# Optimization experiments

Hardware: AMD Instinct MI355X
Metric: run time of the kernel (lower is better)

Reference implementation:

```python
import jax, jax.numpy as jnp
import numpy as np

DEPTH = 8
EMBED = 1280
HEADS = 16
HD = EMBED // HEADS          # 80
MLP = 4 * EMBED              # 5120
HIDDEN = 3584
MERGE = 2
PATCH_DIM = 3 * 2 * 14 * 14  # 1176
THETA = 10000.0


def _layer_norm(x, g, b, eps=1e-6):
    m = jnp.mean(x, -1, keepdims=True)
    v = jnp.mean((x - m) ** 2, -1, keepdims=True)
    return (x - m) * jax.lax.rsqrt(v + eps) * g + b


def _rotate_half(x):
    h = x.shape[-1] // 2
    return jnp.concatenate([-x[..., h:], x[..., :h]], axis=-1)


def _rope_tables(t, h, w):
    # Spatial-merge-ordered h/w position ids (static python ints -> numpy).
    m = MERGE
    hp = np.broadcast_to(np.arange(h)[:, None], (h, w))
    hp = hp.reshape(h // m, m, w // m, m).transpose(0, 2, 1, 3).reshape(-1)
    wp = np.broadcast_to(np.arange(w)[None, :], (h, w))
    wp = wp.reshape(h // m, m, w // m, m).transpose(0, 2, 1, 3).reshape(-1)
    pos = np.tile(np.stack([hp, wp], axis=-1), (t, 1))  # (seq, 2)
    dim = HD // 2
    inv = 1.0 / (THETA ** (np.arange(0, dim, 2, dtype=np.float32) / dim))  # (dim//2,)
    full = np.arange(max(h, w), dtype=np.float32)[:, None] * inv[None, :]  # (max, dim//2)
    emb = full[pos].reshape(pos.shape[0], dim)          # (seq, HD//2)
    emb = np.concatenate([emb, emb], axis=-1)            # (seq, HD)
    return jnp.asarray(np.cos(emb)), jnp.asarray(np.sin(emb))


def setup_inputs() -> dict:
    key = jax.random.key(0)
    ks = jax.random.split(key, 8)
    seq = 1 * 32 * 32
    s = 0.02
    def n(k, shape):
        return jax.random.normal(k, shape, jnp.float32) * s
    return {
        "x": jax.random.normal(ks[0], (seq, PATCH_DIM), jnp.float32),
        "patch_w": n(ks[1], (PATCH_DIM, EMBED)),
        "ln1_g": jnp.ones((DEPTH, EMBED)), "ln1_b": jnp.zeros((DEPTH, EMBED)),
        "qkv_w": n(ks[2], (DEPTH, EMBED, 3 * EMBED)), "qkv_b": jnp.zeros((DEPTH, 3 * EMBED)),
        "proj_w": n(ks[3], (DEPTH, EMBED, EMBED)), "proj_b": jnp.zeros((DEPTH, EMBED)),
        "ln2_g": jnp.ones((DEPTH, EMBED)), "ln2_b": jnp.zeros((DEPTH, EMBED)),
        "fc1_w": n(ks[4], (DEPTH, EMBED, MLP)), "fc1_b": jnp.zeros((DEPTH, MLP)),
        "fc2_w": n(ks[5], (DEPTH, MLP, EMBED)), "fc2_b": jnp.zeros((DEPTH, EMBED)),
        "mln_g": jnp.ones((EMBED,)), "mln_b": jnp.zeros((EMBED,)),
        "mfc1_w": n(ks[6], (EMBED * MERGE ** 2, EMBED * MERGE ** 2)),
        "mfc1_b": jnp.zeros((EMBED * MERGE ** 2,)),
        "mfc2_w": n(ks[7], (EMBED * MERGE ** 2, HIDDEN)),
        "mfc2_b": jnp.zeros((HIDDEN,)),
        "grid_t": 1, "grid_h": 32, "grid_w": 32,
    }


def reference(x, patch_w, ln1_g, ln1_b, qkv_w, qkv_b, proj_w, proj_b,
              ln2_g, ln2_b, fc1_w, fc1_b, fc2_w, fc2_b,
              mln_g, mln_b, mfc1_w, mfc1_b, mfc2_w, mfc2_b,
              grid_t, grid_h, grid_w):
    seq = x.shape[0]
    cos, sin = _rope_tables(int(grid_t), int(grid_h), int(grid_w))  # (seq, HD)
    # Conv3D with kernel == stride == full patch window is a linear projection.
    h = x @ patch_w  # (seq, EMBED)

    def block(h, p):
        l1g, l1b, qw, qb, pw, pb, l2g, l2b, f1w, f1b, f2w, f2b = p
        y = _layer_norm(h, l1g, l1b)
        qkv = (y @ qw + qb).reshape(seq, 3, HEADS, HD)
        q, k, v = qkv[:, 0], qkv[:, 1], qkv[:, 2]  # (seq, HEADS, HD)
        c, si = cos[:, None, :], sin[:, None, :]
        q = q * c + _rotate_half(q) * si
        k = k * c + _rotate_half(k) * si
        attn = jnp.einsum('shd,thd->hst', q, k) * (HD ** -0.5)
        attn = jax.nn.softmax(attn.astype(jnp.float32), axis=-1).astype(h.dtype)
        o = jnp.einsum('hst,thd->shd', attn, v).reshape(seq, EMBED)
        h = h + o @ pw + pb
        y = _layer_norm(h, l2g, l2b)
        y = y @ f1w + f1b
        y = y * jax.nn.sigmoid(1.702 * y)  # quick_gelu
        h = h + y @ f2w + f2b
        return h, None

    h, _ = jax.lax.scan(
        block, h,
        (ln1_g, ln1_b, qkv_w, qkv_b, proj_w, proj_b,
         ln2_g, ln2_b, fc1_w, fc1_b, fc2_w, fc2_b))

    # Patch merger: LN -> group MERGE^2 tokens -> MLP.
    h = _layer_norm(h, mln_g, mln_b)
    h = h.reshape(seq // MERGE ** 2, EMBED * MERGE ** 2)
    h = jax.nn.gelu(h @ mfc1_w + mfc1_b, approximate=True)
    return h @ mfc2_w + mfc2_b  # (seq//4, HIDDEN)
```

## Files before the change

kernel.cpp:

```cpp
#include <hip/hip_runtime.h>
#include <hip/hip_bf16.h>
#include <cmath>

#define SEQ 1024
#define EMBED 1280
#define HEADS 16
#define HD 80
#define HDP 96
#define MLP_DIM 5120
#define HIDDEN 3584
#define QKV3 3840
#define PATCH_DIMS 1176
#define PATCH_PAD 1184
#define DEPTH 8
#define MSEQ 256
#define MDIM 5120
#define KVSPLIT 4

typedef short short8 __attribute__((ext_vector_type(8)));
typedef short short4v __attribute__((ext_vector_type(4)));
typedef float f32x4 __attribute__((ext_vector_type(4)));

#define GLOAD16(g, l)                                                          \
  __builtin_amdgcn_global_load_lds(                                            \
      (const __attribute__((address_space(1))) void*)(g),                      \
      (__attribute__((address_space(3))) void*)(l), 16, 0, 0)

__device__ __forceinline__ float bf2f(unsigned short u) {
  union { unsigned int i; float f; } x;
  x.i = ((unsigned int)u) << 16;
  return x.f;
}
__device__ __forceinline__ unsigned short f2bf(float f) {
  union { float f; unsigned int i; } x;
  x.f = f;
  unsigned int r = x.i + 0x7fffu + ((x.i >> 16) & 1u);
  return (unsigned short)(r >> 16);
}

__device__ inline float waveReduceSum(float v) {
#pragma unroll
  for (int o = 32; o; o >>= 1) v += __shfl_xor(v, o);
  return v;
}

__global__ void rope_tables_kernel(const int* gh_p, const int* gw_p,
                                   float* __restrict__ cosT, float* __restrict__ sinT) {
  int s = blockIdx.x;
  int j = threadIdx.x;
  if (j >= 40) return;
  int gh = *gh_p, gw = *gw_p;
  int f = s % (gh * gw);
  int d0 = f & 1;
  int b = (f >> 1) & 1;
  int rest = f >> 2;
  int W2 = gw >> 1;
  int c = rest % W2;
  int a = rest / W2;
  int hpos = a * 2 + b;
  int wpos = c * 2 + d0;
  int jp = j % 20;
  float inv = powf(10000.0f, -(2.0f * (float)jp) / 40.0f);
  float val = (float)(j < 20 ? hpos : wpos) * inv;
  cosT[s * 40 + j] = cosf(val);
  sinT[s * 40 + j] = sinf(val);
}

__global__ __launch_bounds__(256) void transpose_w(
    const float* __restrict__ W, int ldW, long long wstep,
    unsigned short* __restrict__ Wt, long long tstep, int Ksrc, int Kpad) {
  __shared__ float t[32][132];
  W += (long long)blockIdx.z * wstep;
  Wt += (long long)blockIdx.z * tstep;
  int k0 = blockIdx.x << 7, n0 = blockIdx.y << 5;
#pragma unroll
  for (int i = 0; i < 4; ++i) {
    int flat = threadIdx.x + (i << 8);
    int r = flat >> 3, c4 = (flat & 7) << 2;
    float4 v = make_float4(0.f, 0.f, 0.f, 0.f);
    if (k0 + r < Ksrc) v = *(const float4*)&W[(long long)(k0 + r) * ldW + n0 + c4];
    t[c4][r] = v.x;
    t[c4 + 1][r] = v.y;
    t[c4 + 2][r] = v.z;
    t[c4 + 3][r] = v.w;
  }
  __syncthreads();
  int n = threadIdx.x >> 3, kb = (threadIdx.x & 7) << 2;
#pragma unroll
  for (int j = 0; j < 4; ++j) {
    int k = kb + (j << 5);
    if (k0 + k < Kpad) {
      short4v o;
      o[0] = (short)f2bf(t[n][k]);
      o[1] = (short)f2bf(t[n][k + 1]);
      o[2] = (short)f2bf(t[n][k + 2]);
      o[3] = (short)f2bf(t[n][k + 3]);
      *(short4v*)&Wt[(long long)(n0 + n) * Kpad + k0 + k] = o;
    }
  }
}

__global__ __launch_bounds__(256) void convert_x(const float* __restrict__ x,
                                                 unsigned short* __restrict__ xb) {
  int idx = blockIdx.x * 256 + threadIdx.x;
  if (idx >= SEQ * PATCH_PAD) return;
  int j = idx % PATCH_PAD, s = idx / PATCH_PAD;
  xb[idx] = (j < PATCH_DIMS) ? f2bf(x[(long long)s * PATCH_DIMS + j]) : 0;
}

__global__ __launch_bounds__(256) void gemm_sk(
    const unsigned short* __restrict__ A, int lda,
    const unsigned short* __restrict__ Bt, int ldb,
    void* __restrict__ outp, const float* __restrict__ bias,
    int M, int N, int K, int chunk, int mode) {
  __shared__ short As[128 * 32];
  __shared__ short Bs[128 * 32];
  int nbx = gridDim.x, nby = gridDim.y, nbz = gridDim.z;
  int orig = blockIdx.x + nbx * (blockIdx.y + nby * blockIdx.z);
  int nwg = nbx * nby * nbz;
  int q = nwg >> 3, r = nwg & 7;
  int xcd = orig & 7, pos = orig >> 3;
  int lid = (xcd < r ? xcd * (q + 1) : r * (q + 1) + (xcd - r) * q) + pos;
  int bx = lid % nbx;
  int tt = lid / nbx;
  int by = tt % nby;
  int bz = tt / nby;

  int bm = by << 7, bn = bx << 7;
  int k0 = bz * chunk;
  int kend = min(K, k0 + chunk);
  int tid = threadIdx.x;
  int lane = tid & 63, wid = tid >> 6;
  int wr = wid >> 1, wc = wid & 1;
  f32x4 acc[4][4] = {};

  int arow = (wid << 4) + (lane >> 2);
  int kblk = (lane & 3) << 3;
  const unsigned short* ga = A + (long long)(bm + arow) * lda + k0 + kblk;
  const unsigned short* gb = Bt + (long long)(bn + arow) * ldb + k0 + kblk;
  short* la = &As[arow * 32 + kblk];
  short* lb = &Bs[arow * 32 + kblk];
  long long stepA = 64LL * lda, stepB = 64LL * ldb;

  int l15 = lane & 15, kb8 = (lane >> 4) << 3;
  int rowA = (wr << 6) + l15;
  int rowB = (wc << 6) + l15;

  for (int k = k0; k < kend; k += 32) {
    __syncthreads();
    GLOAD16(ga, la);
    GLOAD16(ga + stepA, la + 64 * 32);
    GLOAD16(gb, lb);
    GLOAD16(gb + stepB, lb + 64 * 32);
    ga += 32;
    gb += 32;
    __syncthreads();
    short8 af[4], bfr[4];
#pragma unroll
    for (int m = 0; m < 4; ++m)
      af[m] = *(const short8*)&As[(rowA + (m << 4)) * 32 + kb8];
#pragma unroll
    for (int n = 0; n < 4; ++n)
      bfr[n] = *(const short8*)&Bs[(rowB + (n << 4)) * 32 + kb8];
#pragma unroll
    for (int m = 0; m < 4; ++m)
#pragma unroll
      for (int n = 0; n < 4; ++n)
        acc[m][n] = __builtin_amdgcn_mfma_f32_16x16x32_bf16(af[m], bfr[n], acc[m][n], 0, 0, 0);
  }

  int lg = lane >> 4;
  float* Cf = (float*)outp + (long long)bz * M * N;
  unsigned short* Cb = (unsigned short*)outp;
#pragma unroll
  for (int m = 0; m < 4; ++m) {
    int row0 = bm + (wr << 6) + (m << 4) + (lg << 2);
#pragma unroll
    for (int n = 0; n < 4; ++n) {
      int col = bn + (wc << 6) + (n << 4) + l15;
      float bval = (mode == 3) ? bias[col] : 0.f;
#pragma unroll
      for (int r2 = 0; r2 < 4; ++r2) {
        int row = row0 + r2;
        float v = acc[m][n][r2];
        if (mode == 0) {
          Cf[(long long)row * N + col] = v;
        } else {
          v += bval;
          Cb[(long long)row * N + col] = f2bf(v / (1.0f + __expf(-1.702f * v)));
        }
      }
    }
  }
}

__global__ __launch_bounds__(256) void reduce_sk(
    const float* __restrict__ P, long long MN, int nsplit,
    const float* __restrict__ bias,
    void* __restrict__ out, int N, int ldout, int colbase, int mode) {
  long long i = ((long long)blockIdx.x * 256 + threadIdx.x) * 4;
  if (i >= MN) return;
  float4 acc = *(const float4*)&P[i];
  for (int s = 1; s < nsplit; ++s) {
    float4 p = *(const float4*)&P[s * MN + i];
    acc.x += p.x; acc.y += p.y; acc.z += p.z; acc.w += p.w;
  }
  int row = (int)(i / N), col = (int)(i % N);
  float v[4] = {acc.x, acc.y, acc.z, acc.w};
  if (bias) {
    float4 bv = *(const float4*)&bias[col];
    v[0] += bv.x; v[1] += bv.y; v[2] += bv.z; v[3] += bv.w;
  }
  long long oi = (long long)row * ldout + colbase + col;
  if (mode == 0) {
    *(float4*)&((float*)out)[oi] = make_float4(v[0], v[1], v[2], v[3]);
  } else if (mode == 3) {
    short4v o;
#pragma unroll
    for (int j = 0; j < 4; ++j)
      o[j] = (short)f2bf(v[j] / (1.0f + __expf(-1.702f * v[j])));
    *(short4v*)&((unsigned short*)out)[oi] = o;
  } else {
    short4v o;
#pragma unroll
    for (int j = 0; j < 4; ++j)
      o[j] = (short)f2bf(0.5f * v[j] * (1.0f + tanhf(0.79788456080286535588f *
                                                     (v[j] + 0.044715f * v[j] * v[j] * v[j]))));
    *(short4v*)&((unsigned short*)out)[oi] = o;
  }
}

__global__ __launch_bounds__(320) void reduce_ln(
    const float* __restrict__ P, int nsplit,
    const float* __restrict__ bias, const float* __restrict__ res,
    const float* __restrict__ g, const float* __restrict__ b,
    float* __restrict__ hout, unsigned short* __restrict__ yout) {
  int r = blockIdx.x, tid = threadIdx.x;
  int c4 = tid << 2;
  const long long MN = (long long)SEQ * EMBED;
  const float* prow = P + (long long)r * EMBED;
  __shared__ float r0[5], r1[5];
  float4 v = make_float4(0.f, 0.f, 0.f, 0.f);
  if (bias) v = *(const float4*)&bias[c4];
  for (int z = 0; z < nsplit; ++z) {
    float4 p = *(const float4*)&prow[(long long)z * MN + c4];
    v.x += p.x; v.y += p.y; v.z += p.z; v.w += p.w;
  }
  if (res) {
    float4 rv = *(const float4*)&res[(long long)r * EMBED + c4];
    v.x += rv.x; v.y += rv.y; v.z += rv.z; v.w += rv.w;
  }
  float s = v.x + v.y + v.z + v.w;
  float sq = v.x * v.x + v.y * v.y + v.z * v.z + v.w * v.w;
  s = waveReduceSum(s);
  sq = waveReduceSum(sq);
  int lane = tid & 63, wid = tid >> 6;
  if (!lane) { r0[wid] = s; r1[wid] = sq; }
  __syncthreads();
  s = r0[0] + r0[1] + r0[2] + r0[3] + r0[4];
  sq = r1[0] + r1[1] + r1[2] + r1[3] + r1[4];
  float mean = s * (1.0f / EMBED);
  float var = sq * (1.0f / EMBED) - mean * mean;
  float rstd = rsqrtf(var + 1e-6f);
  *(float4*)&hout[(long long)r * EMBED + c4] = v;
  float4 gv = *(const float4*)&g[c4];
  float4 bv = *(const float4*)&b[c4];
  short4v o;
  o[0] = (short)f2bf((v.x - mean) * rstd * gv.x + bv.x);
  o[1] = (short)f2bf((v.y - mean) * rstd * gv.y + bv.y);
  o[2] = (short)f2bf((v.z - mean) * rstd * gv.z + bv.z);
  o[3] = (short)f2bf((v.w - mean) * rstd * gv.w + bv.w);
  *(short4v*)&yout[(long long)r * EMBED + c4] = o;
}

__global__ __launch_bounds__(256) void reduce_qkv(
    const float* __restrict__ P, int nsplit,
    const float* __restrict__ bias,
    const float* __restrict__ cosT, const float* __restrict__ sinT,
    unsigned short* __restrict__ qb, unsigned short* __restrict__ kb,
    float qscale) {
  int s = blockIdx.x, tid = threadIdx.x;
  const long long MN = (long long)SEQ * QKV3;
  const float* prow = P + (long long)s * QKV3;
  for (int idx = tid; idx < 640; idx += 256) {
    int hh = idx / 40, j = idx % 40;
    int cq = hh * 80 + j;
    float q0 = bias[cq], q1 = bias[cq + 40];
    float k0 = bias[1280 + cq], k1 = bias[1280 + cq + 40];
    for (int z = 0; z < nsplit; ++z) {
      const float* p = prow + (long long)z * MN;
      q0 += p[cq]; q1 += p[cq + 40];
      k0 += p[1280 + cq]; k1 += p[1280 + cq + 40];
    }
    float cs = cosT[s * 40 + j], sn = sinT[s * 40 + j];
    size_t o = ((size_t)hh * SEQ + s) * HDP;
    qb[o + j] = f2bf((q0 * cs - q1 * sn) * qscale);
    qb[o + j + 40] = f2bf((q1 * cs + q0 * sn) * qscale);
    kb[o + j] = f2bf(k0 * cs - k1 * sn);
    kb[o + j + 40] = f2bf(k1 * cs + k0 * sn);
  }
  {
    int hh = tid >> 4, p = 80 + (tid & 15);
    size_t o = ((size_t)hh * SEQ + s) * HDP + p;
    qb[o] = 0;
    kb[o] = 0;
  }
}

__global__ __launch_bounds__(256) void reduce_packv(
    const float* __restrict__ P, int nsplit, const float* __restrict__ bias,
    unsigned short* __restrict__ vb) {
  __shared__ unsigned short t[80][72];
  int hh = blockIdx.y, s0 = blockIdx.x << 6;
  int tid = threadIdx.x;
  const long long MN = (long long)SEQ * QKV3;
  int s = tid >> 2, c0 = (tid & 3) * 20;
  const float* prow = P + (long long)(s0 + s) * QKV3 + 2560 + hh * 80 + c0;
#pragma unroll
  for (int j = 0; j < 20; ++j) {
    float v = bias[2560 + hh * 80 + c0 + j];
    for (int z = 0; z < nsplit; ++z) v += prow[(long long)z * MN + j];
    t[c0 + j][s] = f2bf(v);
  }
  __syncthreads();
  unsigned short* dst = vb + (size_t)hh * 80 * SEQ + s0;
#pragma unroll
  for (int i = 0; i < 3; ++i) {
    int c = tid + (i << 8);
    if (c < 640) {
      int dr = c >> 3, col = (c & 7) << 3;
      *(short8*)&dst[(size_t)dr * SEQ + col] = *(const short8*)&t[dr][col];
    }
  }
}

__global__ __launch_bounds__(256) void flash_attn_split(
    const unsigned short* __restrict__ qb,
    const unsigned short* __restrict__ kb,
    const unsigned short* __restrict__ vb,
    float* __restrict__ Opart,
    float* __restrict__ mlbuf) {
  __shared__ short Ks[64 * 104];
  __shared__ short Vs[80 * 72];
  __shared__ short Ps[4 * 16 * 72];
  int h = blockIdx.y, q0 = blockIdx.x << 6, z = blockIdx.z;
  int tid = threadIdx.x, lane = tid & 63, wid = tid >> 6;
  int l15 = lane & 15, lg = lane >> 4;
  int kb8 = lg << 3;

  short8 qf[3];
  {
    const unsigned short* qrow = qb + ((size_t)h * SEQ + q0 + (wid << 4) + l15) * HDP;
#pragma unroll
    for (int dc = 0; dc < 3; ++dc) qf[dc] = *(const short8*)&qrow[dc * 32 + kb8];
  }

  f32x4 o_acc[5] = {};
  float m_run = -1e30f, l_run = 0.f;
  short* myP = &Ps[(wid * 16 + l15) * 72];

  const int TPS = 16 / KVSPLIT;
  for (int t = z * TPS; t < z * TPS + TPS; ++t) {
    int kv0 = t << 6;
    __syncthreads();
    {
      const unsigned short* gk = kb + ((size_t)h * SEQ + kv0) * HDP;
#pragma unroll
      for (int i = 0; i < 3; ++i) {
        int c = tid + (i << 8);
        int row = c / 12, col = (c % 12) << 3;
        *(short8*)&Ks[row * 104 + col] = *(const short8*)&gk[row * HDP + col];
      }
      const unsigned short* gv = vb + (size_t)h * 80 * SEQ + kv0;
#pragma unroll
      for (int i = 0; i < 3; ++i) {
        int c = tid + (i << 8);
        if (c < 640) {
          int row = c >> 3, col = (c & 7) << 3;
          *(short8*)&Vs[row * 72 + col] = *(const short8*)&gv[(size_t)row * SEQ + col];
        }
      }
    }
    __syncthreads();

    f32x4 s[4] = {};
#pragma unroll
    for (int ks = 0; ks < 4; ++ks) {
#pragma unroll
      for (int dc = 0; dc < 3; ++dc) {
        short8 kf = *(const short8*)&Ks[(ks * 16 + l15) * 104 + dc * 32 + kb8];
        s[ks] = __builtin_amdgcn_mfma_f32_16x16x32_bf16(kf, qf[dc], s[ks], 0, 0, 0);
      }
    }

    float mloc = -1e30f;
#pragma unroll
    for (int ks = 0; ks < 4; ++ks)
#pragma unroll
      for (int r = 0; r < 4; ++r) mloc = fmaxf(mloc, s[ks][r]);
    mloc = fmaxf(mloc, __shfl_xor(mloc, 16));
    mloc = fmaxf(mloc, __shfl_xor(mloc, 32));
    float m_new = fmaxf(m_run, mloc);
    float alpha = __expf(m_run - m_new);
    float psum = 0.f;
#pragma unroll
    for (int ks = 0; ks < 4; ++ks) {
      short4v pk;
#pragma unroll
      for (int r = 0; r < 4; ++r) {
        float p = __expf(s[ks][r] - m_new);
        psum += p;
        pk[r] = (short)f2bf(p);
      }
      *(short4v*)&myP[ks * 16 + (lg << 2)] = pk;
    }
    psum += __shfl_xor(psum, 16);
    psum += __shfl_xor(psum, 32);
    l_run = l_run * alpha + psum;
    m_run = m_new;
#pragma unroll
    for (int dt = 0; dt < 5; ++dt)
#pragma unroll
      for (int r = 0; r < 4; ++r) o_acc[dt][r] *= alpha;

#pragma unroll
    for (int dt = 0; dt < 5; ++dt) {
#pragma unroll
      for (int kc = 0; kc < 2; ++kc) {
        short8 vf = *(const short8*)&Vs[(dt * 16 + l15) * 72 + kc * 32 + kb8];
        short8 pf = *(const short8*)&myP[kc * 32 + kb8];
        o_acc[dt] = __builtin_amdgcn_mfma_f32_16x16x32_bf16(vf, pf, o_acc[dt], 0, 0, 0);
      }
    }
  }

  int row = q0 + (wid << 4) + l15;
  float* orow = Opart + ((size_t)z * SEQ + row) * EMBED + h * HD;
#pragma unroll
  for (int dt = 0; dt < 5; ++dt)
    *(f32x4*)&orow[dt * 16 + (lg << 2)] = o_acc[dt];
  if (lg == 0) {
    mlbuf[((size_t)(z * 2 + 0) * HEADS + h) * SEQ + row] = m_run;
    mlbuf[((size_t)(z * 2 + 1) * HEADS + h) * SEQ + row] = l_run;
  }
}

__global__ __launch_bounds__(320) void flash_combine(
    const float* __restrict__ Opart, const float* __restrict__ mlbuf,
    unsigned short* __restrict__ ob) {
  int s = blockIdx.x, tid = threadIdx.x;
  __shared__ float ws[KVSPLIT][16], ils[16];
  if (tid < 16) {
    float m = -1e30f;
    float mv[KVSPLIT], lv[KVSPLIT];
#pragma unroll
    for (int z = 0; z < KVSPLIT; ++z) {
      mv[z] = mlbuf[((size_t)(z * 2 + 0) * HEADS + tid) * SEQ + s];
      lv[z] = mlbuf[((size_t)(z * 2 + 1) * HEADS + tid) * SEQ + s];
      m = fmaxf(m, mv[z]);
    }
    float denom = 0.f;
#pragma unroll
    for (int z = 0; z < KVSPLIT; ++z) {
      float w = __expf(mv[z] - m);
      ws[z][tid] = w;
      denom += w * lv[z];
    }
    ils[tid] = 1.0f / denom;
  }
  __syncthreads();
  int c = tid << 2, hh = c / 80;
  float a0 = 0.f, a1 = 0.f, a2 = 0.f, a3 = 0.f;
#pragma unroll
  for (int z = 0; z < KVSPLIT; ++z) {
    float4 o = *(const float4*)&Opart[((size_t)z * SEQ + s) * EMBED + c];
    float w = ws[z][hh];
    a0 += o.x * w; a1 += o.y * w; a2 += o.z * w; a3 += o.w * w;
  }
  float il = ils[hh];
  short4v o;
  o[0] = (short)f2bf(a0 * il);
  o[1] = (short)f2bf(a1 * il);
  o[2] = (short)f2bf(a2 * il);
  o[3] = (short)f2bf(a3 * il);
  *(short4v*)&ob[(size_t)s * EMBED + c] = o;
}

extern "C" void kernel_launch(void* const* d_in, const int* in_sizes, int n_in,
                              void* d_out, int out_size, void* d_ws, size_t ws_size,
                              hipStream_t stream) {
  const float* x = (const float*)d_in[0];
  const float* patch_w = (const float*)d_in[1];
  const float* ln1_g = (const float*)d_in[2];
  const float* ln1_b = (const float*)d_in[3];
  const float* qkv_w = (const float*)d_in[4];
  const float* qkv_b = (const float*)d_in[5];
  const float* proj_w = (const float*)d_in[6];
  const float* proj_b = (const float*)d_in[7];
  const float* ln2_g = (const float*)d_in[8];
  const float* ln2_b = (const float*)d_in[9];
  const float* fc1_w = (const float*)d_in[10];
  const float* fc1_b = (const float*)d_in[11];
  const float* fc2_w = (const float*)d_in[12];
  const float* fc2_b = (const float*)d_in[13];
  const float* mln_g = (const float*)d_in[14];
  const float* mln_b = (const float*)d_in[15];
  const float* mfc1_w = (const float*)d_in[16];
  const float* mfc1_b = (const float*)d_in[17];
  const float* mfc2_w = (const float*)d_in[18];
  const float* mfc2_b = (const float*)d_in[19];
  const int* grid_h = (const int*)d_in[21];
  const int* grid_w = (const int*)d_in[22];

  char* wsp = (char*)d_ws;
  char* ws0 = wsp;
  float* h = (float*)wsp;                       wsp += (size_t)SEQ * EMBED * 4;
  float* cosT = (float*)wsp;                    wsp += (size_t)SEQ * 40 * 4;
  float* sinT = (float*)wsp;                    wsp += (size_t)SEQ * 40 * 4;
  unsigned short* y = (unsigned short*)wsp;     wsp += (size_t)SEQ * EMBED * 2;
  unsigned short* ob = (unsigned short*)wsp;    wsp += (size_t)SEQ * EMBED * 2;
  unsigned short* m1b = (unsigned short*)wsp;   wsp += (size_t)MSEQ * MDIM * 2;
  unsigned short* qb = (unsigned short*)wsp;    wsp += (size_t)HEADS * SEQ * HDP * 2;
  unsigned short* kb = (unsigned short*)wsp;    wsp += (size_t)HEADS * SEQ * HDP * 2;
  unsigned short* vb = (unsigned short*)wsp;    wsp += (size_t)HEADS * HD * SEQ * 2;
  float* Opart = (float*)wsp;                   wsp += (size_t)KVSPLIT * SEQ * EMBED * 4;
  float* mlbuf = (float*)wsp;                   wsp += (size_t)2 * KVSPLIT * HEADS * SEQ * 4;
  unsigned short* u = (unsigned short*)wsp;     wsp += (size_t)SEQ * MLP_DIM * 2;
  unsigned short* xb = (unsigned short*)wsp;    wsp += (size_t)SEQ * PATCH_PAD * 2;
  unsigned short* wt = (unsigned short*)wsp;    wsp += (size_t)(MDIM / 2) * MDIM * 2;
  size_t fixed = (size_t)(wsp - ws0);

  const size_t E_QKV = (size_t)QKV3 * EMBED;
  const size_t E_PROJ = (size_t)EMBED * EMBED;
  const size_t E_FC1 = (size_t)MLP_DIM * EMBED;
  const size_t E_FC2 = (size_t)EMBED * MLP_DIM;
  const size_t E_PATCH = (size_t)EMBED * PATCH_PAD;
  const size_t E_M1 = (size_t)MDIM * MDIM;
  const size_t E_M2 = (size_t)HIDDEN * MDIM;
  size_t wregElems = DEPTH * (E_QKV + E_PROJ + E_FC1 + E_FC2) + E_PATCH + E_M1 + E_M2;
  size_t wregBytes = wregElems * 2;
  bool full = ws_size >= fixed + wregBytes + (size_t)90 * 1024 * 1024;

  unsigned short* wreg = (unsigned short*)wsp;
  unsigned short* Wq = wreg;
  unsigned short* Wp = Wq + DEPTH * E_QKV;
  unsigned short* Wf1 = Wp + DEPTH * E_PROJ;
  unsigned short* Wf2 = Wf1 + DEPTH * E_FC1;
  unsigned short* Wpa = Wf2 + DEPTH * E_FC2;
  unsigned short* Wm1 = Wpa + E_PATCH;
  unsigned short* Wm2 = Wm1 + E_M1;

  float* part = full ? (float*)(wsp + wregBytes) : (float*)wsp;
  size_t avail = ws_size - fixed - (full ? wregBytes : 0);

  auto splits_for = [&](long long MN, int want) {
    size_t one = (size_t)MN * 4;
    if (avail < one) return 1;
    long long cap = (long long)(avail / one);
    return (int)(want < cap ? want : cap);
  };
  auto chunk_for = [](int K, int s) { return ((K + s * 32 - 1) / (s * 32)) * 32; };

  const float scale = 1.0f / sqrtf(80.0f);
  dim3 blk(256);

  rope_tables_kernel<<<SEQ, 64, 0, stream>>>(grid_h, grid_w, cosT, sinT);
  convert_x<<<(SEQ * PATCH_PAD + 255) / 256, blk, 0, stream>>>(x, xb);

  if (full) {
    transpose_w<<<dim3((PATCH_PAD + 127) / 128, EMBED / 32, 1), blk, 0, stream>>>(
        patch_w, EMBED, 0, Wpa, 0, PATCH_DIMS, PATCH_PAD);
    transpose_w<<<dim3(EMBED / 128, QKV3 / 32, DEPTH), blk, 0, stream>>>(
        qkv_w, QKV3, (long long)EMBED * QKV3, Wq, (long long)E_QKV, EMBED, EMBED);
    transpose_w<<<dim3(EMBED / 128, EMBED / 32, DEPTH), blk, 0, stream>>>(
        proj_w, EMBED, (long long)EMBED * EMBED, Wp, (long long)E_PROJ, EMBED, EMBED);
    transpose_w<<<dim3(EMBED / 128, MLP_DIM / 32, DEPTH), blk, 0, stream>>>(
        fc1_w, MLP_DIM, (long long)EMBED * MLP_DIM, Wf1, (long long)E_FC1, EMBED, EMBED);
    transpose_w<<<dim3(MLP_DIM / 128, EMBED / 32, DEPTH), blk, 0, stream>>>(
        fc2_w, EMBED, (long long)MLP_DIM * EMBED, Wf2, (long long)E_FC2, MLP_DIM, MLP_DIM);
    transpose_w<<<dim3(MDIM / 128, MDIM / 32, 1), blk, 0, stream>>>(
        mfc1_w, MDIM, 0, Wm1, 0, MDIM, MDIM);
    transpose_w<<<dim3(MDIM / 128, HIDDEN / 32, 1), blk, 0, stream>>>(
        mfc2_w, HIDDEN, 0, Wm2, 0, MDIM, MDIM);
  }

  {
    const unsigned short* W = Wpa;
    if (!full) {
      transpose_w<<<dim3((PATCH_PAD + 127) / 128, EMBED / 32, 1), blk, 0, stream>>>(
          patch_w, EMBED, 0, wt, 0, PATCH_DIMS, PATCH_PAD);
      W = wt;
    }
    long long MN = (long long)SEQ * EMBED;
    int s = splits_for(MN, 6), ch = chunk_for(PATCH_PAD, s);
    gemm_sk<<<dim3(EMBED / 128, SEQ / 128, s), blk, 0, stream>>>(
        xb, PATCH_PAD, W, PATCH_PAD, part, nullptr, SEQ, EMBED, PATCH_PAD, ch, 0);
    reduce_ln<<<SEQ, 320, 0, stream>>>(part, s, nullptr, nullptr, ln1_g, ln1_b, h, y);
  }

  for (int l = 0; l < DEPTH; ++l) {
    int sq;
    {
      const unsigned short* W = Wq + (size_t)l * E_QKV;
      if (!full) {
        transpose_w<<<dim3(EMBED / 128, QKV3 / 32, 1), blk, 0, stream>>>(
            qkv_w + (long long)l * EMBED * QKV3, QKV3, 0, wt, 0, EMBED, EMBED);
        W = wt;
      }
      long long MN = (long long)SEQ * QKV3;
      sq = splits_for(MN, 2);
      int ch = chunk_for(EMBED, sq);
      gemm_sk<<<dim3(QKV3 / 128, SEQ / 128, sq), blk, 0, stream>>>(
          y, EMBED, W, EMBED, part, nullptr, SEQ, QKV3, EMBED, ch, 0);
      reduce_qkv<<<SEQ, blk, 0, stream>>>(part, sq, qkv_b + l * QKV3,
                                          cosT, sinT, qb, kb, scale);
    }
    reduce_packv<<<dim3(16, HEADS), blk, 0, stream>>>(part, sq, qkv_b + l * QKV3, vb);
    flash_attn_split<<<dim3(SEQ / 64, HEADS, KVSPLIT), blk, 0, stream>>>(
        qb, kb, vb, Opart, mlbuf);
    flash_combine<<<SEQ, 320, 0, stream>>>(Opart, mlbuf, ob);
    {
      const unsigned short* W = Wp + (size_t)l * E_PROJ;
      if (!full) {
        transpose_w<<<dim3(EMBED / 128, EMBED / 32, 1), blk, 0, stream>>>(
            proj_w + (long long)l * EMBED * EMBED, EMBED, 0, wt, 0, EMBED, EMBED);
        W = wt;
      }
      long long MN = (long long)SEQ * EMBED;
      int s = splits_for(MN, 6), ch = chunk_for(EMBED, s);
      gemm_sk<<<dim3(EMBED / 128, SEQ / 128, s), blk, 0, stream>>>(
          ob, EMBED, W, EMBED, part, nullptr, SEQ, EMBED, EMBED, ch, 0);
      reduce_ln<<<SEQ, 320, 0, stream>>>(part, s, proj_b + l * EMBED, h,
                                         ln2_g + l * EMBED, ln2_b + l * EMBED, h, y);
    }
    {
      const unsigned short* W = Wf1 + (size_t)l * E_FC1;
      if (!full) {
        transpose_w<<<dim3(EMBED / 128, MLP_DIM / 32, 1), blk, 0, stream>>>(
            fc1_w + (long long)l * EMBED * MLP_DIM, MLP_DIM, 0, wt, 0, EMBED, EMBED);
        W = wt;
      }
      long long MN = (long long)SEQ * MLP_DIM;
      int s = splits_for(MN, 2), ch = chunk_for(EMBED, s);
      gemm_sk<<<dim3(MLP_DIM / 128, SEQ / 128, s), blk, 0, stream>>>(
          y, EMBED, W, EMBED, part, nullptr, SEQ, MLP_DIM, EMBED, ch, 0);
      reduce_sk<<<(MN / 4 + 255) / 256, blk, 0, stream>>>(
          part, MN, s, fc1_b + l * MLP_DIM, u, MLP_DIM, MLP_DIM, 0, 3);
    }
    {
      const unsigned short* W = Wf2 + (size_t)l * E_FC2;
      if (!full) {
        transpose_w<<<dim3(MLP_DIM / 128, EMBED / 32, 1), blk, 0, stream>>>(
            fc2_w + (long long)l * MLP_DIM * EMBED, EMBED, 0, wt, 0, MLP_DIM, MLP_DIM);
        W = wt;
      }
      long long MN = (long long)SEQ * EMBED;
      int s = splits_for(MN, 8), ch = chunk_for(MLP_DIM, s);
      gemm_sk<<<dim3(EMBED / 128, SEQ / 128, s), blk, 0, stream>>>(
          u, MLP_DIM, W, MLP_DIM, part, nullptr, SEQ, EMBED, MLP_DIM, ch, 0);
      const float* ng = (l < DEPTH - 1) ? ln1_g + (l + 1) * EMBED : mln_g;
      const float* nb = (l < DEPTH - 1) ? ln1_b + (l + 1) * EMBED : mln_b;
      reduce_ln<<<SEQ, 320, 0, stream>>>(part, s, fc2_b + l * EMBED, h, ng, nb, h, y);
    }
  }

  if (full) {
    {
      long long MN = (long long)MSEQ * MDIM;
      int s = splits_for(MN, 12), ch = chunk_for(MDIM, s);
      gemm_sk<<<dim3(MDIM / 128, MSEQ / 128, s), blk, 0, stream>>>(
          y, MDIM, Wm1, MDIM, part, nullptr, MSEQ, MDIM, MDIM, ch, 0);
      reduce_sk<<<(MN / 4 + 255) / 256, blk, 0, stream>>>(
          part, MN, s, mfc1_b, m1b, MDIM, MDIM, 0, 4);
    }
    {
      long long MN = (long long)MSEQ * HIDDEN;
      int s = splits_for(MN, 12), ch = chunk_for(MDIM, s);
      gemm_sk<<<dim3(HIDDEN / 128, MSEQ / 128, s), blk, 0, stream>>>(
          m1b, MDIM, Wm2, MDIM, part, nullptr, MSEQ, HIDDEN, MDIM, ch, 0);
      reduce_sk<<<(MN / 4 + 255) / 256, blk, 0, stream>>>(
          part, MN, s, mfc2_b, (float*)d_out, HIDDEN, HIDDEN, 0, 0);
    }
  } else {
    for (int hh = 0; hh < 2; ++hh) {
      transpose_w<<<dim3(MDIM / 128, 2560 / 32, 1), blk, 0, stream>>>(
          mfc1_w + hh * 2560, MDIM, 0, wt, 0, MDIM, MDIM);
      long long MN = (long long)MSEQ * 2560;
      int s = splits_for(MN, 8), ch = chunk_for(MDIM, s);
      gemm_sk<<<dim3(2560 / 128, MSEQ / 128, s), blk, 0, stream>>>(
          y, MDIM, wt, MDIM, part, nullptr, MSEQ, 2560, MDIM, ch, 0);
      reduce_sk<<<(MN / 4 + 255) / 256, blk, 0, stream>>>(
          part, MN, s, mfc1_b + hh * 2560, m1b, 2560, MDIM, hh * 2560, 4);
    }
    for (int hh = 0; hh < 2; ++hh) {
      transpose_w<<<dim3(MDIM / 128, 1792 / 32, 1), blk, 0, stream>>>(
          mfc2_w + hh * 1792, HIDDEN, 0, wt, 0, MDIM, MDIM);
      long long MN = (long long)MSEQ * 1792;
      int s = splits_for(MN, 8), ch = chunk_for(MDIM, s);
      gemm_sk<<<dim3(1792 / 128, MSEQ / 128, s), blk, 0, stream>>>(
          m1b, MDIM, wt, MDIM, part, nullptr, MSEQ, 1792, MDIM, ch, 0);
      reduce_sk<<<(MN / 4 + 255) / 256, blk, 0, stream>>>(
          part, MN, s, mfc2_b + hh * 1792, (float*)d_out, 1792, HIDDEN, hh * 1792, 0);
    }
  }
}
```

Before: 1.816 ms.

## Store split-K partials in bf16 and merge QKV/V reduction kernels

Split-K GEMM partial sums are now written and read as bf16 instead of fp32, halving the traffic through the partial buffer for every split-K reduction (reduce_sk, reduce_ln, QKV). The separate q/k rope reduction and v pack kernels are merged into one launch with a block-index split, removing one kernel launch per layer. Rounding each partial to bf16 before summation lowers accuracy of the residual stream and layer-norm inputs.

```diff
diff --git a/kernel.cpp b/kernel.cpp
--- a/kernel.cpp
+++ b/kernel.cpp
@@ -170,7 +170,7 @@
   }
 
   int lg = lane >> 4;
-  float* Cf = (float*)outp + (long long)bz * M * N;
+  unsigned short* Cp = (unsigned short*)outp + (long long)bz * M * N;
   unsigned short* Cb = (unsigned short*)outp;
 #pragma unroll
   for (int m = 0; m < 4; ++m) {
@@ -184,7 +184,7 @@
         int row = row0 + r2;
         float v = acc[m][n][r2];
         if (mode == 0) {
-          Cf[(long long)row * N + col] = v;
+          Cp[(long long)row * N + col] = f2bf(v);
         } else {
           v += bval;
           Cb[(long long)row * N + col] = f2bf(v / (1.0f + __expf(-1.702f * v)));
@@ -195,18 +195,18 @@
 }
 
 __global__ __launch_bounds__(256) void reduce_sk(
-    const float* __restrict__ P, long long MN, int nsplit,
+    const unsigned short* __restrict__ P, long long MN, int nsplit,
     const float* __restrict__ bias,
     void* __restrict__ out, int N, int ldout, int colbase, int mode) {
   long long i = ((long long)blockIdx.x * 256 + threadIdx.x) * 4;
   if (i >= MN) return;
-  float4 acc = *(const float4*)&P[i];
-  for (int s = 1; s < nsplit; ++s) {
-    float4 p = *(const float4*)&P[s * MN + i];
-    acc.x += p.x; acc.y += p.y; acc.z += p.z; acc.w += p.w;
+  float v[4] = {0.f, 0.f, 0.f, 0.f};
+  for (int s = 0; s < nsplit; ++s) {
+    short4v p = *(const short4v*)&P[s * MN + i];
+#pragma unroll
+    for (int j = 0; j < 4; ++j) v[j] += bf2f((unsigned short)p[j]);
   }
   int row = (int)(i / N), col = (int)(i % N);
-  float v[4] = {acc.x, acc.y, acc.z, acc.w};
   if (bias) {
     float4 bv = *(const float4*)&bias[col];
     v[0] += bv.x; v[1] += bv.y; v[2] += bv.z; v[3] += bv.w;
@@ -231,20 +231,23 @@
 }
 
 __global__ __launch_bounds__(320) void reduce_ln(
-    const float* __restrict__ P, int nsplit,
+    const unsigned short* __restrict__ P, int nsplit,
     const float* __restrict__ bias, const float* __restrict__ res,
     const float* __restrict__ g, const float* __restrict__ b,
     float* __restrict__ hout, unsigned short* __restrict__ yout) {
   int r = blockIdx.x, tid = threadIdx.x;
   int c4 = tid << 2;
   const long long MN = (long long)SEQ * EMBED;
-  const float* prow = P + (long long)r * EMBED;
+  const unsigned short* prow = P + (long long)r * EMBED;
   __shared__ float r0[5], r1[5];
   float4 v = make_float4(0.f, 0.f, 0.f, 0.f);
   if (bias) v = *(const float4*)&bias[c4];
   for (int z = 0; z < nsplit; ++z) {
-    float4 p = *(const float4*)&prow[(long long)z * MN + c4];
-    v.x += p.x; v.y += p.y; v.z += p.z; v.w += p.w;
+    short4v p = *(const short4v*)&prow[(long long)z * MN + c4];
+    v.x += bf2f((unsigned short)p[0]);
+    v.y += bf2f((unsigned short)p[1]);
+    v.z += bf2f((unsigned short)p[2]);
+    v.w += bf2f((unsigned short)p[3]);
   }
   if (res) {
     float4 rv = *(const float4*)&res[(long long)r * EMBED + c4];
@@ -273,63 +276,62 @@
   *(short4v*)&yout[(long long)r * EMBED + c4] = o;
 }
 
-__global__ __launch_bounds__(256) void reduce_qkv(
-    const float* __restrict__ P, int nsplit,
+__global__ __launch_bounds__(256) void reduce_qkvv(
+    const unsigned short* __restrict__ P, int nsplit,
     const float* __restrict__ bias,
     const float* __restrict__ cosT, const float* __restrict__ sinT,
     unsigned short* __restrict__ qb, unsigned short* __restrict__ kb,
-    float qscale) {
-  int s = blockIdx.x, tid = threadIdx.x;
+    unsigned short* __restrict__ vb, float qscale) {
+  __shared__ unsigned short t[80][72];
+  int b = blockIdx.x, tid = threadIdx.x;
   const long long MN = (long long)SEQ * QKV3;
-  const float* prow = P + (long long)s * QKV3;
-  for (int idx = tid; idx < 640; idx += 256) {
-    int hh = idx / 40, j = idx % 40;
-    int cq = hh * 80 + j;
-    float q0 = bias[cq], q1 = bias[cq + 40];
-    float k0 = bias[1280 + cq], k1 = bias[1280 + cq + 40];
-    for (int z = 0; z < nsplit; ++z) {
-      const float* p = prow + (long long)z * MN;
-      q0 += p[cq]; q1 += p[cq + 40];
-      k0 += p[1280 + cq]; k1 += p[1280 + cq + 40];
-    }
-    float cs = cosT[s * 40 + j], sn = sinT[s * 40 + j];
-    size_t o = ((size_t)hh * SEQ + s) * HDP;
-    qb[o + j] = f2bf((q0 * cs - q1 * sn) * qscale);
-    qb[o + j + 40] = f2bf((q1 * cs + q0 * sn) * qscale);
-    kb[o + j] = f2bf(k0 * cs - k1 * sn);
-    kb[o + j + 40] = f2bf(k1 * cs + k0 * sn);
-  }
-  {
-    int hh = tid >> 4, p = 80 + (tid & 15);
-    size_t o = ((size_t)hh * SEQ + s) * HDP + p;
-    qb[o] = 0;
-    kb[o] = 0;
-  }
-}
-
-__global__ __launch_bounds__(256) void reduce_packv(
-    const float* __restrict__ P, int nsplit, const float* __restrict__ bias,
-    unsigned short* __restrict__ vb) {
-  __shared__ unsigned short t[80][72];
-  int hh = blockIdx.y, s0 = blockIdx.x << 6;
-  int tid = threadIdx.x;
-  const long long MN = (long long)SEQ * QKV3;
-  int s = tid >> 2, c0 = (tid & 3) * 20;
-  const float* prow = P + (long long)(s0 + s) * QKV3 + 2560 + hh * 80 + c0;
-#pragma unroll
-  for (int j = 0; j < 20; ++j) {
-    float v = bias[2560 + hh * 80 + c0 + j];
-    for (int z = 0; z < nsplit; ++z) v += prow[(long long)z * MN + j];
-    t[c0 + j][s] = f2bf(v);
-  }
-  __syncthreads();
-  unsigned short* dst = vb + (size_t)hh * 80 * SEQ + s0;
-#pragma unroll
-  for (int i = 0; i < 3; ++i) {
-    int c = tid + (i << 8);
-    if (c < 640) {
-      int dr = c >> 3, col = (c & 7) << 3;
-      *(short8*)&dst[(size_t)dr * SEQ + col] = *(const short8*)&t[dr][col];
+  if (b < SEQ) {
+    int s = b;
+    const unsigned short* prow = P + (long long)s * QKV3;
+    for (int idx = tid; idx < 640; idx += 256) {
+      int hh = idx / 40, j = idx % 40;
+      int cq = hh * 80 + j;
+      float q0 = bias[cq], q1 = bias[cq + 40];
+      float k0 = bias[1280 + cq], k1 = bias[1280 + cq + 40];
+      for (int z = 0; z < nsplit; ++z) {
+        const unsigned short* p = prow + (long long)z * MN;
+        q0 += bf2f(p[cq]); q1 += bf2f(p[cq + 40]);
+        k0 += bf2f(p[1280 + cq]); k1 += bf2f(p[1280 + cq + 40]);
+      }
+      float cs = cosT[s * 40 + j], sn = sinT[s * 40 + j];
+      size_t o = ((size_t)hh * SEQ + s) * HDP;
+      qb[o + j] = f2bf((q0 * cs - q1 * sn) * qscale);
+      qb[o + j + 40] = f2bf((q1 * cs + q0 * sn) * qscale);
+      kb[o + j] = f2bf(k0 * cs - k1 * sn);
+      kb[o + j + 40] = f2bf(k1 * cs + k0 * sn);
+    }
+    {
+      int hh = tid >> 4, p = 80 + (tid & 15);
+      size_t o = ((size_t)hh * SEQ + s) * HDP + p;
+      qb[o] = 0;
+      kb[o] = 0;
+    }
+  } else {
+    int bb = b - SEQ;
+    int hh = bb >> 4, s0 = (bb & 15) << 6;
+    int s = tid >> 2, c0 = (tid & 3) * 20;
+    const unsigned short* prow =
+        P + (long long)(s0 + s) * QKV3 + 2560 + hh * 80 + c0;
+#pragma unroll
+    for (int j = 0; j < 20; ++j) {
+      float v = bias[2560 + hh * 80 + c0 + j];
+      for (int z = 0; z < nsplit; ++z) v += bf2f(prow[(long long)z * MN + j]);
+      t[c0 + j][s] = f2bf(v);
+    }
+    __syncthreads();
+    unsigned short* dst = vb + (size_t)hh * 80 * SEQ + s0;
+#pragma unroll
+    for (int i = 0; i < 3; ++i) {
+      int c = tid + (i << 8);
+      if (c < 640) {
+        int dr = c >> 3, col = (c & 7) << 3;
+        *(short8*)&dst[(size_t)dr * SEQ + col] = *(const short8*)&t[dr][col];
+      }
     }
   }
 }
@@ -550,11 +552,12 @@
   unsigned short* Wm1 = Wpa + E_PATCH;
   unsigned short* Wm2 = Wm1 + E_M1;
 
-  float* part = full ? (float*)(wsp + wregBytes) : (float*)wsp;
+  unsigned short* part =
+      full ? (unsigned short*)(wsp + wregBytes) : (unsigned short*)wsp;
   size_t avail = ws_size - fixed - (full ? wregBytes : 0);
 
   auto splits_for = [&](long long MN, int want) {
-    size_t one = (size_t)MN * 4;
+    size_t one = (size_t)MN * 2;
     if (avail < one) return 1;
     long long cap = (long long)(avail / one);
     return (int)(want < cap ? want : cap);
@@ -612,10 +615,9 @@
       int ch = chunk_for(EMBED, sq);
       gemm_sk<<<dim3(QKV3 / 128, SEQ / 128, sq), blk, 0, stream>>>(
           y, EMBED, W, EMBED, part, nullptr, SEQ, QKV3, EMBED, ch, 0);
-      reduce_qkv<<<SEQ, blk, 0, stream>>>(part, sq, qkv_b + l * QKV3,
-                                          cosT, sinT, qb, kb, scale);
-    }
-    reduce_packv<<<dim3(16, HEADS), blk, 0, stream>>>(part, sq, qkv_b + l * QKV3, vb);
+      reduce_qkvv<<<SEQ + 16 * HEADS, blk, 0, stream>>>(
+          part, sq, qkv_b + l * QKV3, cosT, sinT, qb, kb, vb, scale);
+    }
     flash_attn_split<<<dim3(SEQ / 64, HEADS, KVSPLIT), blk, 0, stream>>>(
         qb, kb, vb, Opart, mlbuf);
     flash_combine<<<SEQ, 320, 0, stream>>>(Opart, mlbuf, ob);
```

Result: faster. 1.651 ms (-9.1%).
